# Kernel tuning notes

Measured on AMD Instinct MI355X. Metric: run time of the kernel, lower is better.

## Reference

```python
import jax, jax.numpy as jnp
import numpy as np

B, S, D, H = 512, 200, 512, 8
FF = 1024          # dim_feedforward == hidden_dim
EMB, HID, FIN = 128, 1024, 64
V = 100000
QK_SCALE, ATTN_CLIP, FFN_CLIP, QKV_CLIP = 0.05, 3.0, 2.0, 1.0
PAD = 0


def _ln(x, g, b, eps=1e-6):
    m = jnp.mean(x, -1, keepdims=True)
    v = jnp.mean((x - m) ** 2, -1, keepdims=True)
    return (x - m) / jnp.sqrt(v + eps) * g + b


def setup_inputs() -> dict:
    key = jax.random.key(0)
    ks = jax.random.split(key, 32)
    n = lambda i, shape, s=0.02: (s * jax.random.normal(ks[i], shape)).astype(jnp.float32)
    emb_table = n(0, (V, D)).at[PAD].set(0.0)  # padding row zeroed
    inp = {
        'item_seq': jax.random.randint(ks[20], (B, S), 0, V),
        'user_avg_ctr': jax.random.uniform(ks[21], (B,)),
        'user_total_interactions': jax.random.uniform(ks[22], (B,)),
        'age_price': jax.random.randint(ks[23], (B,), 0, 100),
        'gender_cate': jax.random.randint(ks[24], (B,), 0, 10),
        'cms_group_id': jax.random.randint(ks[25], (B,), 0, 13),
        'emb_table': emb_table,
        'in_proj_w': n(1, (3 * D, D)),
        'out_proj_w': n(2, (D, D)),
        'out_proj_b': jnp.zeros((D,), jnp.float32),
        'ln1_g': jnp.ones((D,), jnp.float32), 'ln1_b': jnp.zeros((D,), jnp.float32),
        'ln2_g': jnp.ones((D,), jnp.float32), 'ln2_b': jnp.zeros((D,), jnp.float32),
        'lin1_w': n(3, (FF, D)), 'lin1_b': jnp.zeros((FF,), jnp.float32),
        'lin2_w': n(4, (D, FF)), 'lin2_b': jnp.zeros((D,), jnp.float32),
        'age_tab': n(5, (100, EMB)), 'gender_tab': n(6, (10, EMB)), 'cms_tab': n(7, (13, EMB)),
        'ctr_w': n(8, (EMB, 1)), 'ctr_b': jnp.zeros((EMB,), jnp.float32),
        'ti_w': n(9, (EMB, 1)), 'ti_b': jnp.zeros((EMB,), jnp.float32),
        'mlp1_w': n(10, (HID, D + 5 * EMB)), 'mlp1_b': jnp.zeros((HID,), jnp.float32),
        'mlp2_w': n(11, (FIN, HID)), 'mlp2_b': jnp.zeros((FIN,), jnp.float32),
    }
    return inp


def reference(item_seq, user_avg_ctr, user_total_interactions, age_price, gender_cate,
              cms_group_id, emb_table, in_proj_w, out_proj_w, out_proj_b,
              ln1_g, ln1_b, ln2_g, ln2_b, lin1_w, lin1_b, lin2_w, lin2_b,
              age_tab, gender_tab, cms_tab, ctr_w, ctr_b, ti_w, ti_b,
              mlp1_w, mlp1_b, mlp2_w, mlp2_b):
    dk = D // H
    pad = item_seq == PAD  # [B,S] key padding mask
    x = jnp.clip(emb_table[item_seq] * 0.5, -1.0, 1.0)  # [B,S,D]

    # ---- custom self-attention block (no in_proj bias, heavy clamping) ----
    qw, kw, vw = in_proj_w[:D], in_proj_w[D:2 * D], in_proj_w[2 * D:]
    q = jnp.clip(x @ qw.T, -QKV_CLIP, QKV_CLIP)
    k = jnp.clip(x @ kw.T, -QKV_CLIP, QKV_CLIP)
    v = jnp.clip(x @ vw.T, -QKV_CLIP, QKV_CLIP)
    q = q.reshape(B, S, H, dk).transpose(0, 2, 1, 3)
    k = k.reshape(B, S, H, dk).transpose(0, 2, 1, 3)
    v = v.reshape(B, S, H, dk).transpose(0, 2, 1, 3)
    scores = jnp.einsum('bhqd,bhkd->bhqk', q, k) / (np.float32(np.sqrt(dk)) * QK_SCALE)
    scores = jnp.clip(scores, -ATTN_CLIP, ATTN_CLIP)
    scores = jnp.where(pad[:, None, None, :], -1e9, scores)
    w = jax.nn.softmax(scores, axis=-1)  # dropout is identity in eval
    x2 = jnp.einsum('bhqk,bhkd->bhqd', w, v).transpose(0, 2, 1, 3).reshape(B, S, D)
    x2 = jnp.clip(x2 @ out_proj_w.T + out_proj_b, -ATTN_CLIP, ATTN_CLIP)
    sa = _ln(x + x2, ln1_g, ln1_b)          # norm1 inside overridden _sa_block
    x = _ln(x + sa, ln1_g, ln1_b)           # base post-norm wraps norm1 again

    # ---- FFN block with clamps ----
    h = jax.nn.relu(jnp.clip(x @ lin1_w.T + lin1_b, -FFN_CLIP, FFN_CLIP))
    f2 = jnp.clip(h @ lin2_w.T + lin2_b, -FFN_CLIP, FFN_CLIP)
    ff = _ln(x + f2, ln2_g, ln2_b)          # norm2 inside overridden _ff_block
    x = _ln(x + ff, ln2_g, ln2_b)           # base wraps norm2 again

    seq_out = jnp.clip(x, -5.0, 5.0)
    m = (~pad).astype(seq_out.dtype)[:, :, None]
    seq_rep = jnp.clip((seq_out * m).sum(1) / (m.sum(1) + 1e-8), -5.0, 5.0)  # [B,D]

    ape = age_tab[age_price]
    ge = gender_tab[gender_cate]
    ce = cms_tab[cms_group_id]
    ctr = user_avg_ctr[:, None] @ ctr_w.T + ctr_b
    ti = user_total_interactions[:, None] @ ti_w.T + ti_b
    u = jnp.concatenate([seq_rep, ctr, ti, ape, ge, ce], axis=-1)  # [B, D+5*EMB]
    return jax.nn.relu(u @ mlp1_w.T + mlp1_b) @ mlp2_w.T + mlp2_b  # [B, FIN]
```

## Files before the change

kernel.cpp:

```cpp
#include <hip/hip_runtime.h>
#include <hip/hip_bf16.h>
#include <stdint.h>

typedef __attribute__((ext_vector_type(8))) short short8;
typedef __attribute__((ext_vector_type(4))) float f32x4;
typedef unsigned short u16;

#define MFMA16(a,b,c) __builtin_amdgcn_mfma_f32_16x16x32_bf16((a),(b),(c),0,0,0)

__device__ __forceinline__ u16 f2bf(float f) {
  unsigned int u = __float_as_uint(f);
  return (u16)((u + 0x7FFFu + ((u >> 16) & 1u)) >> 16);
}
__device__ __forceinline__ float bf2f(u16 h) {
  return __uint_as_float(((unsigned int)h) << 16);
}
__device__ __forceinline__ float clampf(float v, float lo, float hi) {
  return fminf(fmaxf(v, lo), hi);
}
__device__ __forceinline__ void gl2lds16(const u16* g, u16* l) {
  __builtin_amdgcn_global_load_lds(
      (const __attribute__((address_space(1))) unsigned int*)g,
      (__attribute__((address_space(3))) unsigned int*)(uintptr_t)l,
      16, 0, 0);
}

__global__ __launch_bounds__(256) void cvt_bf16_kernel(
    const float* __restrict__ src, u16* __restrict__ dst, int n) {
  for (int i = blockIdx.x*256 + threadIdx.x; i < n; i += gridDim.x*256)
    dst[i] = f2bf(src[i]);
}

__global__ __launch_bounds__(256) void embed_kernel(
    const int* __restrict__ iseq, const float* __restrict__ emb,
    u16* __restrict__ xb) {
  int gid = blockIdx.x*256 + threadIdx.x;
  int m = gid >> 7;
  int c = (gid & 127) * 4;
  int item = iseq[m];
  float4 e = *(const float4*)&emb[(size_t)item*512 + c];
  ushort4 hb;
  hb.x = f2bf(clampf(e.x*0.5f, -1.f, 1.f));
  hb.y = f2bf(clampf(e.y*0.5f, -1.f, 1.f));
  hb.z = f2bf(clampf(e.z*0.5f, -1.f, 1.f));
  hb.w = f2bf(clampf(e.w*0.5f, -1.f, 1.f));
  *(ushort4*)&xb[(size_t)m*512 + c] = hb;
}

__global__ __launch_bounds__(256) void cnt_kernel(
    const int* __restrict__ item_seq, float* __restrict__ cnt) {
  __shared__ int sred[4];
  int b = blockIdx.x, tid = threadIdx.x;
  int lane = tid & 63, wv = tid >> 6;
  int c = 0;
  if (tid < 200) c = (item_seq[b*200 + tid] != 0) ? 1 : 0;
  #pragma unroll
  for (int m = 1; m <= 32; m <<= 1) c += __shfl_xor(c, m);
  if (lane == 0) sred[wv] = c;
  __syncthreads();
  if (tid == 0) cnt[b] = (float)(sred[0]+sred[1]+sred[2]+sred[3]);
}

#define BAR() asm volatile("s_barrier" ::: "memory")

__device__ __forceinline__ void stage_half(const char* gsrc0, size_t rstride,
                                           u16* lhalf, int wv, int lane) {
  #pragma unroll
  for (int j = 0; j < 2; ++j) {
    const int o   = j*8192 + wv*1024 + lane*16;
    const int row = o >> 7;
    const int cb  = (o & 127) ^ ((row & 7) << 4);
    gl2lds16((const u16*)(gsrc0 + (size_t)row*rstride + cb),
             (u16*)((char*)lhalf + j*8192 + wv*1024));
  }
}

__device__ __forceinline__ short8 ldsfrag(const u16* slot, int row, int kb) {
  return *(const short8*)((const char*)slot + row*128 + (kb ^ ((row & 7) << 4)));
}

#define QUAD(AH, NB)                                                          \
  _Pragma("unroll")                                                           \
  for (int i = 0; i < 4; ++i)                                                 \
    _Pragma("unroll")                                                         \
    for (int nf = 0; nf < 2; ++nf)                                            \
      _Pragma("unroll")                                                       \
      for (int ks = 0; ks < 2; ++ks)                                          \
        acc[(AH)*4 + i][(NB)*2 + nf] =                                        \
            MFMA16(af[AH][i][ks], bf[nf][ks], acc[(AH)*4 + i][(NB)*2 + nf]);

template <int MODE>
__global__ __launch_bounds__(512)
void gemm_bt(const u16* __restrict__ A, const u16* __restrict__ Bw,
             const float* __restrict__ bias, int K, int Nt, int swz,
             u16* __restrict__ outB, u16* __restrict__ QKV, long long projStride) {
  __shared__ __align__(16) u16 As[2][256*64];
  __shared__ __align__(16) u16 Bs[2][256*64];
  const int tid  = threadIdx.x;
  const int lane = tid & 63;
  const int wv   = tid >> 6;
  const int wm   = wv >> 2;
  const int wn   = wv & 3;
  const int id   = blockIdx.x;
  int mt, nt2;
  if (swz) { mt = (id / (8*Nt))*8 + (id & 7); nt2 = (id >> 3) % Nt; }
  else     { mt = id / Nt;                    nt2 = id % Nt; }
  const int m0 = mt * 256;
  const int n0 = nt2 * 256;
  const int KT = K >> 6;

  const char* Abase = (const char*)(A  + (size_t)m0*K);
  const char* Bbase = (const char*)(Bw + (size_t)n0*K);
  const size_t rs = (size_t)K * 2;

  const int r16 = lane & 15;
  const int q4  = lane >> 4;

  const f32x4 fz = {0.f, 0.f, 0.f, 0.f};
  f32x4 acc[8][4];
  #pragma unroll
  for (int i = 0; i < 8; ++i)
    #pragma unroll
    for (int j = 0; j < 4; ++j) acc[i][j] = fz;

  stage_half(Abase,            rs, &As[0][0],      wv, lane);
  stage_half(Abase + 128*rs,   rs, &As[0][128*64], wv, lane);
  stage_half(Bbase,            rs, &Bs[0][0],      wv, lane);
  stage_half(Bbase + 128*rs,   rs, &Bs[0][128*64], wv, lane);
  if (KT > 1) {
    stage_half(Abase + 128,          rs, &As[1][0],      wv, lane);
    stage_half(Abase + 128*rs + 128, rs, &As[1][128*64], wv, lane);
    asm volatile("s_waitcnt vmcnt(4)" ::: "memory");
  } else {
    asm volatile("s_waitcnt vmcnt(0)" ::: "memory");
  }
  BAR();

  short8 af[2][4][2];
  short8 bf[2][2];

  for (int t = 0; t < KT; ++t) {
    const int cur = t & 1;
    const u16* Asl = As[cur];
    const u16* Bsl = Bs[cur];
    u16* Bnx = Bs[cur ^ 1];
    u16* Anx = As[cur];
    const char* Bg1 = Bbase + (size_t)(t+1)*128;
    const char* Ag2 = Abase + (size_t)(t+2)*128;
    const bool s1 = (t+1 < KT);
    const bool s2 = (t+2 < KT);

    #pragma unroll
    for (int i = 0; i < 4; ++i)
      #pragma unroll
      for (int ks = 0; ks < 2; ++ks)
        af[0][i][ks] = ldsfrag(Asl, wm*128 + i*16 + r16, ks*64 + q4*16);
    #pragma unroll
    for (int nf = 0; nf < 2; ++nf)
      #pragma unroll
      for (int ks = 0; ks < 2; ++ks)
        bf[nf][ks] = ldsfrag(Bsl, wn*64 + nf*16 + r16, ks*64 + q4*16);
    if (s1) stage_half(Bg1, rs, Bnx, wv, lane);
    BAR();
    __builtin_amdgcn_s_setprio(1);
    QUAD(0, 0);
    __builtin_amdgcn_s_setprio(0);
    BAR();

    #pragma unroll
    for (int i = 0; i < 4; ++i)
      #pragma unroll
      for (int ks = 0; ks < 2; ++ks)
        af[1][i][ks] = ldsfrag(Asl, wm*128 + 64 + i*16 + r16, ks*64 + q4*16);
    if (s1) stage_half(Bg1 + 128*rs, rs, Bnx + 128*64, wv, lane);
    BAR();
    __builtin_amdgcn_s_setprio(1);
    QUAD(1, 0);
    __builtin_amdgcn_s_setprio(0);
    BAR();

    #pragma unroll
    for (int nf = 0; nf < 2; ++nf)
      #pragma unroll
      for (int ks = 0; ks < 2; ++ks)
        bf[nf][ks] = ldsfrag(Bsl, wn*64 + 32 + nf*16 + r16, ks*64 + q4*16);
    if (s2) stage_half(Ag2, rs, Anx, wv, lane);
    BAR();
    __builtin_amdgcn_s_setprio(1);
    QUAD(1, 1);
    __builtin_amdgcn_s_setprio(0);
    BAR();

    if (s2) stage_half(Ag2 + 128*rs, rs, Anx + 128*64, wv, lane);
    if (t < KT-2)       asm volatile("s_waitcnt vmcnt(4)" ::: "memory");
    else if (t == KT-2) asm volatile("s_waitcnt vmcnt(0)" ::: "memory");
    BAR();
    __builtin_amdgcn_s_setprio(1);
    QUAD(0, 1);
    __builtin_amdgcn_s_setprio(0);
    BAR();
  }

  if (MODE == 0) {
    #pragma unroll
    for (int nf = 0; nf < 4; ++nf) {
      const int col = n0 + wn*64 + nf*16 + r16;
      const unsigned proj = (unsigned)col >> 9;
      const unsigned hh   = ((unsigned)col >> 6) & 7u;
      const unsigned dk   = (unsigned)col & 63u;
      u16* base = QKV + (size_t)proj*projStride + (size_t)hh*12800 + dk;
      #pragma unroll
      for (int mi = 0; mi < 8; ++mi) {
        const int rowb = m0 + wm*128 + mi*16 + q4*4;
        int b = rowb / 200;
        int s = rowb - b*200;
        size_t addr = (size_t)b*102400 + (size_t)s*64;
        #pragma unroll
        for (int r = 0; r < 4; ++r) {
          base[addr] = f2bf(clampf(acc[mi][nf][r], -1.f, 1.f));
          ++s; addr += 64;
          if (s == 200) { s = 0; addr += 102400 - 12800; }
        }
      }
    }
  } else {
    const int N = (MODE == 2) ? 1024 : 512;
    #pragma unroll
    for (int nf = 0; nf < 4; ++nf) {
      const int col = n0 + wn*64 + nf*16 + r16;
      const float bvs = bias[col];
      #pragma unroll
      for (int mi = 0; mi < 8; ++mi) {
        const int rowb = m0 + wm*128 + mi*16 + q4*4;
        #pragma unroll
        for (int r = 0; r < 4; ++r) {
          const int row = rowb + r;
          float v = acc[mi][nf][r] + bvs;
          if (MODE == 1)      v = clampf(v, -3.f, 3.f);
          else if (MODE == 2) v = fmaxf(clampf(v, -2.f, 2.f), 0.f);
          else                v = clampf(v, -2.f, 2.f);
          outB[(size_t)row*N + col] = f2bf(v);
        }
      }
    }
  }
}

__global__ __launch_bounds__(512)
void attn_kernel(const u16* __restrict__ Q, const u16* __restrict__ K,
                 const u16* __restrict__ V, const int* __restrict__ iseq,
                 u16* __restrict__ x2b) {
  __shared__ __align__(16) u16 Ks[208*72];
  __shared__ __align__(16) u16 Vs[64*232];
  __shared__ __align__(16) u16 Ps[8][16*40];
  __shared__ float msk[208];

  const int tid = threadIdx.x, lane = tid & 63, wv = tid >> 6;
  const unsigned bid = blockIdx.x;
  const int h = bid & 7;
  const int b = bid >> 3;
  const size_t bh = (size_t)b*8 + h;
  const u16* Kg = K + bh*12800;
  const u16* Vg = V + bh*12800;
  const u16* Qg = Q + bh*12800;

  for (int c = tid; c < 3200; c += 512) {
    int row = c >> 4, q = c & 15;
    *(ushort4*)&Ks[row*72 + q*4] = *(const ushort4*)&Kg[row*64 + q*4];
  }
  {
    const int quad = wv*2 + (lane >> 5);
    const int sl   = lane & 31;
    #pragma unroll
    for (int it = 0; it < 7; ++it) {
      const int s = sl + it*32;
      if (s < 200) {
        ushort4 v4 = *(const ushort4*)&Vg[s*64 + quad*4];
        Vs[(quad*4+0)*232 + s] = v4.x;
        Vs[(quad*4+1)*232 + s] = v4.y;
        Vs[(quad*4+2)*232 + s] = v4.z;
        Vs[(quad*4+3)*232 + s] = v4.w;
      }
    }
  }
  for (int c = tid; c < 2048; c += 512) {
    int dk = c >> 5, s2 = 200 + (c & 31);
    Vs[dk*232 + s2] = 0;
  }
  for (int t = tid; t < 208; t += 512)
    msk[t] = (t < 200 && iseq[b*200 + t] != 0) ? 1.f : 0.f;
  __syncthreads();

  const int colk = lane & 15;
  const int fk8 = (lane >> 4) * 8;
  const int prow = (lane >> 4) * 4;
  const f32x4 fz = {0.f,0.f,0.f,0.f};

  for (int qb = 0; qb < 2; ++qb) {
    const int qrow = qb*128 + wv*16 + (lane & 15);
    const int qsrc = qrow < 200 ? qrow : 199;
    short8 qa0 = *(const short8*)&Qg[(size_t)qsrc*64 + fk8];
    short8 qa1 = *(const short8*)&Qg[(size_t)qsrc*64 + 32 + fk8];
    f32x4 oacc[4];
    #pragma unroll
    for (int nt = 0; nt < 4; ++nt) oacc[nt] = fz;
    float rs[4] = {0.f,0.f,0.f,0.f};

    for (int kt2 = 0; kt2 < 7; ++kt2) {
      #pragma unroll
      for (int half = 0; half < 2; ++half) {
        const int stile = kt2*2 + half;
        if (stile < 13) {
          const int key = stile*16 + colk;
          short8 kb0 = *(const short8*)&Ks[key*72 + fk8];
          short8 kb1 = *(const short8*)&Ks[key*72 + 32 + fk8];
          f32x4 sc = fz;
          __builtin_amdgcn_s_setprio(1);
          sc = MFMA16(qa0, kb0, sc);
          sc = MFMA16(qa1, kb1, sc);
          __builtin_amdgcn_s_setprio(0);
          const float mk = msk[key];
          #pragma unroll
          for (int r = 0; r < 4; ++r) {
            float p = __expf(clampf(sc[r]*2.5f, -3.f, 3.f)) * mk;
            rs[r] += p;
            Ps[wv][(prow + r)*40 + half*16 + colk] = f2bf(p);
          }
        } else {
          #pragma unroll
          for (int r = 0; r < 4; ++r)
            Ps[wv][(prow + r)*40 + half*16 + colk] = 0;
        }
      }
      asm volatile("s_waitcnt lgkmcnt(0)" ::: "memory");
      short8 pa = *(const short8*)&Ps[wv][(lane & 15)*40 + fk8];
      const int kb32 = kt2*32;
      __builtin_amdgcn_s_setprio(1);
      #pragma unroll
      for (int nt = 0; nt < 4; ++nt) {
        short8 vb = *(const short8*)&Vs[(nt*16 + colk)*232 + kb32 + fk8];
        oacc[nt] = MFMA16(pa, vb, oacc[nt]);
      }
      __builtin_amdgcn_s_setprio(0);
      asm volatile("s_waitcnt lgkmcnt(0)" ::: "memory");
    }

    #pragma unroll
    for (int m = 1; m <= 8; m <<= 1)
      #pragma unroll
      for (int r = 0; r < 4; ++r) rs[r] += __shfl_xor(rs[r], m);

    const int srow = qb*128 + wv*16 + prow;
    #pragma unroll
    for (int r = 0; r < 4; ++r) {
      const int s = srow + r;
      if (s < 200) {
        const float inv = rs[r] > 0.f ? 1.f/rs[r] : 0.f;
        const size_t base = ((size_t)b*200 + s)*512 + h*64;
        #pragma unroll
        for (int nt = 0; nt < 4; ++nt)
          x2b[base + nt*16 + colk] = f2bf(oacc[nt][r] * inv);
      }
    }
  }
}

__global__ __launch_bounds__(256)
void ln1_kernel(const u16* __restrict__ xb, const u16* __restrict__ x2b,
                const float* __restrict__ g, const float* __restrict__ bb,
                u16* __restrict__ xnb) {
  const int lane = threadIdx.x & 63, wv = threadIdx.x >> 6;
  const size_t t = (size_t)blockIdx.x*4 + wv;
  const int c0 = lane*4, c1 = 256 + lane*4;
  ushort4 xa = *(const ushort4*)&xb[t*512 + c0];
  ushort4 xc = *(const ushort4*)&xb[t*512 + c1];
  ushort4 ha = *(const ushort4*)&x2b[t*512 + c0];
  ushort4 hc = *(const ushort4*)&x2b[t*512 + c1];
  float xv[8] = {bf2f(xa.x),bf2f(xa.y),bf2f(xa.z),bf2f(xa.w),
                 bf2f(xc.x),bf2f(xc.y),bf2f(xc.z),bf2f(xc.w)};
  float tv[8] = {xv[0]+bf2f(ha.x), xv[1]+bf2f(ha.y), xv[2]+bf2f(ha.z), xv[3]+bf2f(ha.w),
                 xv[4]+bf2f(hc.x), xv[5]+bf2f(hc.y), xv[6]+bf2f(hc.z), xv[7]+bf2f(hc.w)};
  float s1 = 0.f, s2 = 0.f;
  #pragma unroll
  for (int i = 0; i < 8; ++i) { s1 += tv[i]; s2 += tv[i]*tv[i]; }
  #pragma unroll
  for (int m = 1; m <= 32; m <<= 1) { s1 += __shfl_xor(s1, m); s2 += __shfl_xor(s2, m); }
  float mean = s1*(1.f/512.f);
  float inv = 1.f/sqrtf(s2*(1.f/512.f) - mean*mean + 1e-6f);
  float4 ga = *(const float4*)(g + c0), gc = *(const float4*)(g + c1);
  float4 ba = *(const float4*)(bb + c0), bc = *(const float4*)(bb + c1);
  float gv[8] = {ga.x,ga.y,ga.z,ga.w, gc.x,gc.y,gc.z,gc.w};
  float bv[8] = {ba.x,ba.y,ba.z,ba.w, bc.x,bc.y,bc.z,bc.w};
  float uv[8]; float s3 = 0.f, s4 = 0.f;
  #pragma unroll
  for (int i = 0; i < 8; ++i) {
    float sa = (tv[i]-mean)*inv*gv[i] + bv[i];
    uv[i] = xv[i] + sa;
    s3 += uv[i]; s4 += uv[i]*uv[i];
  }
  #pragma unroll
  for (int m = 1; m <= 32; m <<= 1) { s3 += __shfl_xor(s3, m); s4 += __shfl_xor(s4, m); }
  float mean2 = s3*(1.f/512.f);
  float inv2 = 1.f/sqrtf(s4*(1.f/512.f) - mean2*mean2 + 1e-6f);
  ushort4 o0, o1;
  o0.x = f2bf((uv[0]-mean2)*inv2*gv[0] + bv[0]);
  o0.y = f2bf((uv[1]-mean2)*inv2*gv[1] + bv[1]);
  o0.z = f2bf((uv[2]-mean2)*inv2*gv[2] + bv[2]);
  o0.w = f2bf((uv[3]-mean2)*inv2*gv[3] + bv[3]);
  o1.x = f2bf((uv[4]-mean2)*inv2*gv[4] + bv[4]);
  o1.y = f2bf((uv[5]-mean2)*inv2*gv[5] + bv[5]);
  o1.z = f2bf((uv[6]-mean2)*inv2*gv[6] + bv[6]);
  o1.w = f2bf((uv[7]-mean2)*inv2*gv[7] + bv[7]);
  *(ushort4*)&xnb[t*512 + c0] = o0;
  *(ushort4*)&xnb[t*512 + c1] = o1;
}

__global__ __launch_bounds__(256)
void ln2_kernel(const u16* __restrict__ xnb, const u16* __restrict__ f2b,
                const float* __restrict__ g, const float* __restrict__ bb,
                const int* __restrict__ iseq, float* __restrict__ seq_acc) {
  const int tid = threadIdx.x, lane = tid & 63, wv = tid >> 6;
  const int q = blockIdx.x, bl = blockIdx.y;
  const int c8 = lane*8;
  float gv[8], bv[8];
  *(float4*)&gv[0] = *(const float4*)(g + c8);
  *(float4*)&gv[4] = *(const float4*)(g + c8 + 4);
  *(float4*)&bv[0] = *(const float4*)(bb + c8);
  *(float4*)&bv[4] = *(const float4*)(bb + c8 + 4);
  float acc[8] = {};
  for (int i = wv; i < 50; i += 4) {
    const int s = q*50 + i;
    const size_t row = (size_t)bl*200 + s;
    short8 xh = *(const short8*)&xnb[row*512 + c8];
    short8 yh = *(const short8*)&f2b[row*512 + c8];
    float xv[8], tv[8];
    #pragma unroll
    for (int j = 0; j < 8; ++j) {
      xv[j] = bf2f((u16)xh[j]);
      tv[j] = xv[j] + bf2f((u16)yh[j]);
    }
    float s1 = 0.f, s2 = 0.f;
    #pragma unroll
    for (int j = 0; j < 8; ++j) { s1 += tv[j]; s2 += tv[j]*tv[j]; }
    #pragma unroll
    for (int m = 1; m <= 32; m <<= 1) { s1 += __shfl_xor(s1,m); s2 += __shfl_xor(s2,m); }
    float mean = s1*(1.f/512.f);
    float inv = 1.f/sqrtf(s2*(1.f/512.f) - mean*mean + 1e-6f);
    float uv[8]; float s3 = 0.f, s4 = 0.f;
    #pragma unroll
    for (int j = 0; j < 8; ++j) {
      uv[j] = xv[j] + (tv[j]-mean)*inv*gv[j] + bv[j];
      s3 += uv[j]; s4 += uv[j]*uv[j];
    }
    #pragma unroll
    for (int m = 1; m <= 32; m <<= 1) { s3 += __shfl_xor(s3,m); s4 += __shfl_xor(s4,m); }
    float mean2 = s3*(1.f/512.f);
    float inv2 = 1.f/sqrtf(s4*(1.f/512.f) - mean2*mean2 + 1e-6f);
    if (iseq[row] != 0) {
      #pragma unroll
      for (int j = 0; j < 8; ++j)
        acc[j] += clampf((uv[j]-mean2)*inv2*gv[j] + bv[j], -5.f, 5.f);
    }
  }
  float* dst = &seq_acc[(((size_t)bl*4 + q)*4 + wv)*512 + c8];
  *(float4*)&dst[0] = *(float4*)&acc[0];
  *(float4*)&dst[4] = *(float4*)&acc[4];
}

__global__ __launch_bounds__(256)
void build_u_kernel(const float* __restrict__ seq_acc, const float* __restrict__ cnt,
                    const float* __restrict__ uac, const float* __restrict__ uti,
                    const int* __restrict__ age, const int* __restrict__ gen,
                    const int* __restrict__ cms,
                    const float* __restrict__ age_tab, const float* __restrict__ gen_tab,
                    const float* __restrict__ cms_tab,
                    const float* __restrict__ ctr_w, const float* __restrict__ ctr_b,
                    const float* __restrict__ ti_w, const float* __restrict__ ti_b,
                    float* __restrict__ u) {
  const int b = blockIdx.x;
  for (int j = threadIdx.x; j < 1152; j += 256) {
    float v;
    if (j < 512) {
      float ssum = 0.f;
      #pragma unroll
      for (int p = 0; p < 16; ++p) ssum += seq_acc[((size_t)b*16 + p)*512 + j];
      v = clampf(ssum / (cnt[b] + 1e-8f), -5.f, 5.f);
    }
    else if (j < 640)  { int e = j-512;  v = uac[b]*ctr_w[e] + ctr_b[e]; }
    else if (j < 768)  { int e = j-640;  v = uti[b]*ti_w[e] + ti_b[e]; }
    else if (j < 896)  { int e = j-768;  v = age_tab[age[b]*128 + e]; }
    else if (j < 1024) { int e = j-896;  v = gen_tab[gen[b]*128 + e]; }
    else               { int e = j-1024; v = cms_tab[cms[b]*128 + e]; }
    u[(size_t)b*1152 + j] = v;
  }
}

__global__ __launch_bounds__(256)
void mlp1_kernel(const float* __restrict__ u, const float* __restrict__ w,
                 const float* __restrict__ bias, float* __restrict__ h1) {
  __shared__ __align__(16) float As[64][36];
  __shared__ __align__(16) float Wt[32][68];
  const int tid = threadIdx.x;
  const int m0 = blockIdx.x*64, n0 = blockIdx.y*64;
  const int tm = tid >> 4, tn = tid & 15;
  float acc[4][4] = {};
  for (int k0 = 0; k0 < 1152; k0 += 32) {
    for (int c = tid; c < 512; c += 256) {
      int row = c >> 3, q = c & 7;
      *(float4*)&As[row][q*4] = *(const float4*)&u[(size_t)(m0+row)*1152 + k0 + q*4];
      float4 wv4 = *(const float4*)&w[(size_t)(n0+row)*1152 + k0 + q*4];
      Wt[q*4+0][row] = wv4.x; Wt[q*4+1][row] = wv4.y;
      Wt[q*4+2][row] = wv4.z; Wt[q*4+3][row] = wv4.w;
    }
    __syncthreads();
    #pragma unroll
    for (int kk = 0; kk < 32; ++kk) {
      float av[4], bw[4];
      #pragma unroll
      for (int i = 0; i < 4; ++i) av[i] = As[tm*4+i][kk];
      #pragma unroll
      for (int j = 0; j < 4; ++j) bw[j] = Wt[kk][tn*4+j];
      #pragma unroll
      for (int i = 0; i < 4; ++i)
        #pragma unroll
        for (int j = 0; j < 4; ++j) acc[i][j] += av[i]*bw[j];
    }
    __syncthreads();
  }
  #pragma unroll
  for (int i = 0; i < 4; ++i)
    #pragma unroll
    for (int j = 0; j < 4; ++j) {
      int n = n0 + tn*4 + j;
      h1[(size_t)(m0 + tm*4 + i)*1024 + n] = fmaxf(acc[i][j] + bias[n], 0.f);
    }
}

__global__ __launch_bounds__(256)
void mlp2_kernel(const float* __restrict__ h1, const float* __restrict__ w,
                 const float* __restrict__ bias, float* __restrict__ out) {
  const int tid = threadIdx.x;
  const int m = blockIdx.x*4 + (tid >> 6);
  const int n = tid & 63;
  const float4* hr = (const float4*)(h1 + (size_t)m*1024);
  const float4* wr = (const float4*)(w + (size_t)n*1024);
  float acc = 0.f;
  for (int k4 = 0; k4 < 256; ++k4) {
    float4 a = hr[k4], bw = wr[k4];
    acc += a.x*bw.x + a.y*bw.y + a.z*bw.z + a.w*bw.w;
  }
  out[(size_t)m*64 + n] = acc + bias[n];
}

extern "C" void kernel_launch(void* const* d_in, const int* in_sizes, int n_in,
                              void* d_out, int out_size, void* d_ws, size_t ws_size,
                              hipStream_t stream) {
  (void)in_sizes; (void)n_in; (void)out_size;
  const int*   item_seq   = (const int*)d_in[0];
  const float* uac        = (const float*)d_in[1];
  const float* uti        = (const float*)d_in[2];
  const int*   age        = (const int*)d_in[3];
  const int*   gen        = (const int*)d_in[4];
  const int*   cms        = (const int*)d_in[5];
  const float* emb        = (const float*)d_in[6];
  const float* in_proj_w  = (const float*)d_in[7];
  const float* out_proj_w = (const float*)d_in[8];
  const float* out_proj_b = (const float*)d_in[9];
  const float* ln1_g = (const float*)d_in[10];
  const float* ln1_b = (const float*)d_in[11];
  const float* ln2_g = (const float*)d_in[12];
  const float* ln2_b = (const float*)d_in[13];
  const float* lin1_w = (const float*)d_in[14];
  const float* lin1_b = (const float*)d_in[15];
  const float* lin2_w = (const float*)d_in[16];
  const float* lin2_b = (const float*)d_in[17];
  const float* age_tab = (const float*)d_in[18];
  const float* gen_tab = (const float*)d_in[19];
  const float* cms_tab = (const float*)d_in[20];
  const float* ctr_w = (const float*)d_in[21];
  const float* ctr_b = (const float*)d_in[22];
  const float* ti_w  = (const float*)d_in[23];
  const float* ti_b  = (const float*)d_in[24];
  const float* mlp1_w = (const float*)d_in[25];
  const float* mlp1_b = (const float*)d_in[26];
  const float* mlp2_w = (const float*)d_in[27];
  const float* mlp2_b = (const float*)d_in[28];

  const long long TAILB = 25430016LL;
  int CB = 32;
  if      ((long long)ws_size >= 512LL*1024000 + TAILB) CB = 512;
  else if ((long long)ws_size >= 128LL*1024000 + TAILB) CB = 128;
  else if ((long long)ws_size >=  64LL*1024000 + TAILB) CB = 64;
  const long long R = (long long)CB * 204800;

  char* ws = (char*)d_ws;
  u16* xb   = (u16*)(ws);
  u16* x2b  = (u16*)(ws + R);
  u16* Qb   = (u16*)(ws + 2*R);
  u16* Kb   = (u16*)(ws + 3*R);
  u16* Vrb  = (u16*)(ws + 4*R);
  u16* x2o  = Qb;
  u16* xnb  = Kb;
  u16* f2b  = Vrb;
  u16* hbuf = (u16*)(ws);
  char* tail = ws + 5*R;
  float* seq_acc = (float*)(tail);
  float* cnt     = (float*)(tail + 16777216);
  float* u       = (float*)(tail + 16779264);
  float* h1      = (float*)(tail + 19138560);
  u16*   wqkv    = (u16*)(tail + 21235712);
  u16*   wout    = (u16*)(tail + 22808576);
  u16*   wl1     = (u16*)(tail + 23332864);
  u16*   wl2     = (u16*)(tail + 24381440);

  cvt_bf16_kernel<<<768, 256, 0, stream>>>(in_proj_w, wqkv, 1536*512);
  cvt_bf16_kernel<<<256, 256, 0, stream>>>(out_proj_w, wout, 512*512);
  cvt_bf16_kernel<<<512, 256, 0, stream>>>(lin1_w, wl1, 1024*512);
  cvt_bf16_kernel<<<512, 256, 0, stream>>>(lin2_w, wl2, 512*1024);
  cnt_kernel<<<512, 256, 0, stream>>>(item_seq, cnt);

  const int nch = 512 / CB;
  const int Mc  = CB * 200;
  const int Mt  = Mc / 256;
  const int swz = (Mt % 8 == 0) ? 1 : 0;
  const long long projStride = (long long)CB * 102400;
  for (int ch = 0; ch < nch; ++ch) {
    const int* iseq = item_seq + (size_t)ch*CB*200;
    embed_kernel<<<Mc/2, 256, 0, stream>>>(iseq, emb, xb);
    gemm_bt<0><<<Mt*6, 512, 0, stream>>>(xb, wqkv, nullptr, 512, 6, swz,
                                         nullptr, Qb, projStride);
    attn_kernel<<<CB*8, 512, 0, stream>>>(Qb, Kb, Vrb, iseq, x2b);
    gemm_bt<1><<<Mt*2, 512, 0, stream>>>(x2b, wout, out_proj_b, 512, 2, swz,
                                         x2o, nullptr, 0);
    ln1_kernel<<<Mc/4, 256, 0, stream>>>(xb, x2o, ln1_g, ln1_b, xnb);
    gemm_bt<2><<<Mt*4, 512, 0, stream>>>(xnb, wl1, lin1_b, 512, 4, swz,
                                         hbuf, nullptr, 0);
    gemm_bt<3><<<Mt*2, 512, 0, stream>>>(hbuf, wl2, lin2_b, 1024, 2, swz,
                                         f2b, nullptr, 0);
    ln2_kernel<<<dim3(4, CB), 256, 0, stream>>>(xnb, f2b, ln2_g, ln2_b, iseq,
                                                seq_acc + (size_t)ch*CB*8192);
  }

  build_u_kernel<<<512, 256, 0, stream>>>(seq_acc, cnt, uac, uti, age, gen, cms,
                                          age_tab, gen_tab, cms_tab,
                                          ctr_w, ctr_b, ti_w, ti_b, u);
  mlp1_kernel<<<dim3(8, 16), 256, 0, stream>>>(u, mlp1_w, mlp1_b, h1);
  mlp2_kernel<<<128, 256, 0, stream>>>(h1, mlp2_w, mlp2_b, (float*)d_out);
}
```

Before: 1.432 ms.

## Software-pipeline A fragment loads across iterations and halve GEMM barriers

Restructures the bf16 MFMA GEMM main loop. The first A fragments for the next k-tile are now loaded from the other LDS buffer at the end of each iteration, global-to-LDS staging is issued earlier, and the number of s_barriers per k-step drops from eight to four, with sched_barrier fences in between. It also adds a min-blocks hint of 2 to launch_bounds, which tightens the register budget and may cause spills. The next-tile A fragments are read after only a per-wave vmcnt wait and before a barrier, so the code risks reading LDS that other waves have not finished staging.

After: 1.437 ms. No clear change (+0.3%).

```diff
diff --git a/kernel.cpp b/kernel.cpp
--- a/kernel.cpp
+++ b/kernel.cpp
@@ -62,6 +62,7 @@
 }
 
 #define BAR() asm volatile("s_barrier" ::: "memory")
+#define SCHEDB() __builtin_amdgcn_sched_barrier(0)
 
 __device__ __forceinline__ void stage_half(const char* gsrc0, size_t rstride,
                                            u16* lhalf, int wv, int lane) {
@@ -79,18 +80,8 @@
   return *(const short8*)((const char*)slot + row*128 + (kb ^ ((row & 7) << 4)));
 }
 
-#define QUAD(AH, NB)                                                          \
-  _Pragma("unroll")                                                           \
-  for (int i = 0; i < 4; ++i)                                                 \
-    _Pragma("unroll")                                                         \
-    for (int nf = 0; nf < 2; ++nf)                                            \
-      _Pragma("unroll")                                                       \
-      for (int ks = 0; ks < 2; ++ks)                                          \
-        acc[(AH)*4 + i][(NB)*2 + nf] =                                        \
-            MFMA16(af[AH][i][ks], bf[nf][ks], acc[(AH)*4 + i][(NB)*2 + nf]);
-
 template <int MODE>
-__global__ __launch_bounds__(512)
+__global__ __launch_bounds__(512, 2)
 void gemm_bt(const u16* __restrict__ A, const u16* __restrict__ Bw,
              const float* __restrict__ bias, int K, int Nt, int swz,
              u16* __restrict__ outB, u16* __restrict__ QKV, long long projStride) {
@@ -123,6 +114,8 @@
     #pragma unroll
     for (int j = 0; j < 4; ++j) acc[i][j] = fz;
 
+  short8 af0[4][2], af1[4][2], bflo[2][2], bfhi[2][2];
+
   stage_half(Abase,            rs, &As[0][0],      wv, lane);
   stage_half(Abase + 128*rs,   rs, &As[0][128*64], wv, lane);
   stage_half(Bbase,            rs, &Bs[0][0],      wv, lane);
@@ -135,69 +128,108 @@
     asm volatile("s_waitcnt vmcnt(0)" ::: "memory");
   }
   BAR();
-
-  short8 af[2][4][2];
-  short8 bf[2][2];
+  #pragma unroll
+  for (int i = 0; i < 4; ++i)
+    #pragma unroll
+    for (int ks = 0; ks < 2; ++ks)
+      af0[i][ks] = ldsfrag(&As[0][0], wm*128 + i*16 + r16, ks*64 + q4*16);
 
   for (int t = 0; t < KT; ++t) {
     const int cur = t & 1;
     const u16* Asl = As[cur];
     const u16* Bsl = Bs[cur];
-    u16* Bnx = Bs[cur ^ 1];
-    u16* Anx = As[cur];
+    const u16* Asn = As[cur ^ 1];
+    u16* Bnx = (u16*)As[0];
+    Bnx = (u16*)Bs[cur ^ 1];
+    u16* Anx = (u16*)As[cur];
     const char* Bg1 = Bbase + (size_t)(t+1)*128;
     const char* Ag2 = Abase + (size_t)(t+2)*128;
     const bool s1 = (t+1 < KT);
     const bool s2 = (t+2 < KT);
 
+    if (s1) stage_half(Bg1, rs, Bnx, wv, lane);
+    if (t == KT-1) {
+      #pragma unroll
+      for (int i = 0; i < 4; ++i)
+        #pragma unroll
+        for (int ks = 0; ks < 2; ++ks)
+          af0[i][ks] = ldsfrag(Asl, wm*128 + i*16 + r16, ks*64 + q4*16);
+    }
+    #pragma unroll
+    for (int nf = 0; nf < 2; ++nf)
+      #pragma unroll
+      for (int ks = 0; ks < 2; ++ks)
+        bflo[nf][ks] = ldsfrag(Bsl, wn*64 + nf*16 + r16, ks*64 + q4*16);
     #pragma unroll
     for (int i = 0; i < 4; ++i)
       #pragma unroll
       for (int ks = 0; ks < 2; ++ks)
-        af[0][i][ks] = ldsfrag(Asl, wm*128 + i*16 + r16, ks*64 + q4*16);
+        af1[i][ks] = ldsfrag(Asl, wm*128 + 64 + i*16 + r16, ks*64 + q4*16);
+    __builtin_amdgcn_s_setprio(1);
+    #pragma unroll
+    for (int i = 0; i < 4; ++i)
+      #pragma unroll
+      for (int nf = 0; nf < 2; ++nf)
+        #pragma unroll
+        for (int ks = 0; ks < 2; ++ks)
+          acc[i][nf] = MFMA16(af0[i][ks], bflo[nf][ks], acc[i][nf]);
+    __builtin_amdgcn_s_setprio(0);
+    SCHEDB();
+    BAR();
+
+    if (s1) stage_half(Bg1 + 128*rs, rs, Bnx + 128*64, wv, lane);
     #pragma unroll
     for (int nf = 0; nf < 2; ++nf)
       #pragma unroll
       for (int ks = 0; ks < 2; ++ks)
-        bf[nf][ks] = ldsfrag(Bsl, wn*64 + nf*16 + r16, ks*64 + q4*16);
-    if (s1) stage_half(Bg1, rs, Bnx, wv, lane);
+        bfhi[nf][ks] = ldsfrag(Bsl, wn*64 + 32 + nf*16 + r16, ks*64 + q4*16);
+    __builtin_amdgcn_s_setprio(1);
+    #pragma unroll
+    for (int i = 0; i < 4; ++i)
+      #pragma unroll
+      for (int nf = 0; nf < 2; ++nf)
+        #pragma unroll
+        for (int ks = 0; ks < 2; ++ks)
+          acc[4+i][nf] = MFMA16(af1[i][ks], bflo[nf][ks], acc[4+i][nf]);
+    __builtin_amdgcn_s_setprio(0);
+    SCHEDB();
     BAR();
+
+    if (s2) stage_half(Ag2, rs, Anx, wv, lane);
+    if (t < KT-2) asm volatile("s_waitcnt vmcnt(6)" ::: "memory");
     __builtin_amdgcn_s_setprio(1);
-    QUAD(0, 0);
+    #pragma unroll
+    for (int i = 0; i < 4; ++i)
+      #pragma unroll
+      for (int nf = 0; nf < 2; ++nf)
+        #pragma unroll
+        for (int ks = 0; ks < 2; ++ks)
+          acc[4+i][2+nf] = MFMA16(af1[i][ks], bfhi[nf][ks], acc[4+i][2+nf]);
     __builtin_amdgcn_s_setprio(0);
+    SCHEDB();
     BAR();
 
+    if (s2) stage_half(Ag2 + 128*rs, rs, Anx + 128*64, wv, lane);
+    __builtin_amdgcn_s_setprio(1);
     #pragma unroll
     for (int i = 0; i < 4; ++i)
       #pragma unroll
-      for (int ks = 0; ks < 2; ++ks)
-        af[1][i][ks] = ldsfrag(Asl, wm*128 + 64 + i*16 + r16, ks*64 + q4*16);
-    if (s1) stage_half(Bg1 + 128*rs, rs, Bnx + 128*64, wv, lane);
-    BAR();
-    __builtin_amdgcn_s_setprio(1);
-    QUAD(1, 0);
+      for (int nf = 0; nf < 2; ++nf)
+        #pragma unroll
+        for (int ks = 0; ks < 2; ++ks)
+          acc[i][2+nf] = MFMA16(af0[i][ks], bfhi[nf][ks], acc[i][2+nf]);
     __builtin_amdgcn_s_setprio(0);
-    BAR();
-
-    #pragma unroll
-    for (int nf = 0; nf < 2; ++nf)
-      #pragma unroll
-      for (int ks = 0; ks < 2; ++ks)
-        bf[nf][ks] = ldsfrag(Bsl, wn*64 + 32 + nf*16 + r16, ks*64 + q4*16);
-    if (s2) stage_half(Ag2, rs, Anx, wv, lane);
-    BAR();
-    __builtin_amdgcn_s_setprio(1);
-    QUAD(1, 1);
-    __builtin_amdgcn_s_setprio(0);
-    BAR();
-
-    if (s2) stage_half(Ag2 + 128*rs, rs, Anx + 128*64, wv, lane);
-    if (t < KT-2)       asm volatile("s_waitcnt vmcnt(4)" ::: "memory");
-    else if (t == KT-2) asm volatile("s_waitcnt vmcnt(0)" ::: "memory");
-    BAR();
-    __builtin_amdgcn_s_setprio(1);
-    QUAD(0, 1);
-    __builtin_amdgcn_s_setprio(0);
+    if (t < KT-2) {
+      asm volatile("s_waitcnt vmcnt(4)" ::: "memory");
+      #pragma unroll
+      for (int i = 0; i < 4; ++i)
+        #pragma unroll
+        for (int ks = 0; ks < 2; ++ks)
+          af0[i][ks] = ldsfrag(Asn, wm*128 + i*16 + r16, ks*64 + q4*16);
+    } else if (t == KT-2) {
+      asm volatile("s_waitcnt vmcnt(0)" ::: "memory");
+    }
+    SCHEDB();
     BAR();
   }
 
```

## Unroll GEMM K-loop by two with explicit waitcnt scheduling and static buffers

Applied to the files above, without the earlier changes.

Restructures the 8-wave 256x256 GEMM main loop to process two K-tiles per iteration so LDS buffer indices are compile-time constants. It inserts explicit lgkmcnt/vmcnt waits and sched barriers around each MFMA quadrant to interleave LDS reads, global-to-LDS staging and MFMA issue more tightly. It also adds a min-blocks hint to launch_bounds. The unrolled loop assumes KT is even, and the rewritten wait placement risks stalls or races if the vmcnt accounting is off.

After: 1.422 ms. About the same (-0.7%).

```diff
diff --git a/kernel.cpp b/kernel.cpp
--- a/kernel.cpp
+++ b/kernel.cpp
@@ -62,6 +62,10 @@
 }
 
 #define BAR() asm volatile("s_barrier" ::: "memory")
+#define LGKM0() do { asm volatile("s_waitcnt lgkmcnt(0)" ::: "memory"); \
+                     __builtin_amdgcn_sched_barrier(0); } while (0)
+#define VM4() asm volatile("s_waitcnt vmcnt(4)" ::: "memory")
+#define VM0() asm volatile("s_waitcnt vmcnt(0)" ::: "memory")
 
 __device__ __forceinline__ void stage_half(const char* gsrc0, size_t rstride,
                                            u16* lhalf, int wv, int lane) {
@@ -89,8 +93,22 @@
         acc[(AH)*4 + i][(NB)*2 + nf] =                                        \
             MFMA16(af[AH][i][ks], bf[nf][ks], acc[(AH)*4 + i][(NB)*2 + nf]);
 
+#define RD_AF(H, SLOT)                                                        \
+  _Pragma("unroll")                                                           \
+  for (int i = 0; i < 4; ++i)                                                 \
+    _Pragma("unroll")                                                         \
+    for (int ks = 0; ks < 2; ++ks)                                            \
+      af[H][i][ks] = ldsfrag((SLOT), wm*128 + (H)*64 + i*16 + r16, ks*64 + q4*16);
+
+#define RD_BF(SLOT, OFF)                                                      \
+  _Pragma("unroll")                                                           \
+  for (int nf = 0; nf < 2; ++nf)                                              \
+    _Pragma("unroll")                                                         \
+    for (int ks = 0; ks < 2; ++ks)                                            \
+      bf[nf][ks] = ldsfrag((SLOT), wn*64 + (OFF) + nf*16 + r16, ks*64 + q4*16);
+
 template <int MODE>
-__global__ __launch_bounds__(512)
+__global__ __launch_bounds__(512, 2)
 void gemm_bt(const u16* __restrict__ A, const u16* __restrict__ Bw,
              const float* __restrict__ bias, int K, int Nt, int swz,
              u16* __restrict__ outB, u16* __restrict__ QKV, long long projStride) {
@@ -108,6 +126,7 @@
   const int m0 = mt * 256;
   const int n0 = nt2 * 256;
   const int KT = K >> 6;
+  const int NI = KT >> 1;
 
   const char* Abase = (const char*)(A  + (size_t)m0*K);
   const char* Bbase = (const char*)(Bw + (size_t)n0*K);
@@ -123,82 +142,74 @@
     #pragma unroll
     for (int j = 0; j < 4; ++j) acc[i][j] = fz;
 
-  stage_half(Abase,            rs, &As[0][0],      wv, lane);
-  stage_half(Abase + 128*rs,   rs, &As[0][128*64], wv, lane);
-  stage_half(Bbase,            rs, &Bs[0][0],      wv, lane);
-  stage_half(Bbase + 128*rs,   rs, &Bs[0][128*64], wv, lane);
-  if (KT > 1) {
-    stage_half(Abase + 128,          rs, &As[1][0],      wv, lane);
-    stage_half(Abase + 128*rs + 128, rs, &As[1][128*64], wv, lane);
-    asm volatile("s_waitcnt vmcnt(4)" ::: "memory");
-  } else {
-    asm volatile("s_waitcnt vmcnt(0)" ::: "memory");
-  }
-  BAR();
-
   short8 af[2][4][2];
   short8 bf[2][2];
 
-  for (int t = 0; t < KT; ++t) {
-    const int cur = t & 1;
-    const u16* Asl = As[cur];
-    const u16* Bsl = Bs[cur];
-    u16* Bnx = Bs[cur ^ 1];
-    u16* Anx = As[cur];
-    const char* Bg1 = Bbase + (size_t)(t+1)*128;
-    const char* Ag2 = Abase + (size_t)(t+2)*128;
-    const bool s1 = (t+1 < KT);
-    const bool s2 = (t+2 < KT);
-
-    #pragma unroll
-    for (int i = 0; i < 4; ++i)
-      #pragma unroll
-      for (int ks = 0; ks < 2; ++ks)
-        af[0][i][ks] = ldsfrag(Asl, wm*128 + i*16 + r16, ks*64 + q4*16);
-    #pragma unroll
-    for (int nf = 0; nf < 2; ++nf)
-      #pragma unroll
-      for (int ks = 0; ks < 2; ++ks)
-        bf[nf][ks] = ldsfrag(Bsl, wn*64 + nf*16 + r16, ks*64 + q4*16);
-    if (s1) stage_half(Bg1, rs, Bnx, wv, lane);
+  stage_half(Abase,              rs, &As[0][0],      wv, lane);
+  stage_half(Abase + 128*rs,     rs, &As[0][128*64], wv, lane);
+  stage_half(Bbase,              rs, &Bs[0][0],      wv, lane);
+  stage_half(Bbase + 128*rs,     rs, &Bs[0][128*64], wv, lane);
+  stage_half(Abase + 128,        rs, &As[1][0],      wv, lane);
+  stage_half(Abase + 128*rs + 128, rs, &As[1][128*64], wv, lane);
+  VM4();
+  BAR();
+
+  for (int it = 0; it < NI; ++it) {
+    const int ta = it*2;
+    const bool m2 = (ta + 2 < KT);
+    const char* gBb  = Bbase + (size_t)(ta+1)*128;
+    const char* gAa2 = Abase + (size_t)(ta+2)*128;
+    const char* gBa2 = Bbase + (size_t)(ta+2)*128;
+    const char* gAb1 = Abase + (size_t)(ta+3)*128;
+
+    RD_AF(0, As[0]); RD_BF(Bs[0], 0);
+    asm volatile("s_waitcnt lgkmcnt(8)" ::: "memory");
+    stage_half(gBb, rs, &Bs[1][0], wv, lane);
+    BAR(); LGKM0();
+    __builtin_amdgcn_s_setprio(1); QUAD(0, 0); __builtin_amdgcn_s_setprio(0);
+    VM4(); BAR();
+
+    RD_AF(1, As[0]);
+    stage_half(gBb + 128*rs, rs, &Bs[1][128*64], wv, lane);
+    BAR(); LGKM0();
+    __builtin_amdgcn_s_setprio(1); QUAD(1, 0); __builtin_amdgcn_s_setprio(0);
+    VM4(); BAR();
+
+    RD_BF(Bs[0], 32);
+    if (m2) stage_half(gAa2, rs, &As[0][0], wv, lane);
+    BAR(); LGKM0();
+    __builtin_amdgcn_s_setprio(1); QUAD(1, 1); __builtin_amdgcn_s_setprio(0);
+    VM4(); BAR();
+
+    if (m2) stage_half(gAa2 + 128*rs, rs, &As[0][128*64], wv, lane);
     BAR();
-    __builtin_amdgcn_s_setprio(1);
-    QUAD(0, 0);
-    __builtin_amdgcn_s_setprio(0);
+    __builtin_amdgcn_s_setprio(1); QUAD(0, 1); __builtin_amdgcn_s_setprio(0);
+    if (m2) { VM4(); } else { VM0(); }
     BAR();
 
-    #pragma unroll
-    for (int i = 0; i < 4; ++i)
-      #pragma unroll
-      for (int ks = 0; ks < 2; ++ks)
-        af[1][i][ks] = ldsfrag(Asl, wm*128 + 64 + i*16 + r16, ks*64 + q4*16);
-    if (s1) stage_half(Bg1 + 128*rs, rs, Bnx + 128*64, wv, lane);
+    RD_AF(0, As[1]); RD_BF(Bs[1], 0);
+    asm volatile("s_waitcnt lgkmcnt(8)" ::: "memory");
+    if (m2) stage_half(gBa2, rs, &Bs[0][0], wv, lane);
+    BAR(); LGKM0();
+    __builtin_amdgcn_s_setprio(1); QUAD(0, 0); __builtin_amdgcn_s_setprio(0);
+    VM4(); BAR();
+
+    RD_AF(1, As[1]);
+    if (m2) stage_half(gBa2 + 128*rs, rs, &Bs[0][128*64], wv, lane);
+    BAR(); LGKM0();
+    __builtin_amdgcn_s_setprio(1); QUAD(1, 0); __builtin_amdgcn_s_setprio(0);
+    VM4(); BAR();
+
+    RD_BF(Bs[1], 32);
+    if (m2) stage_half(gAb1, rs, &As[1][0], wv, lane);
+    BAR(); LGKM0();
+    __builtin_amdgcn_s_setprio(1); QUAD(1, 1); __builtin_amdgcn_s_setprio(0);
+    VM4(); BAR();
+
+    if (m2) stage_half(gAb1 + 128*rs, rs, &As[1][128*64], wv, lane);
     BAR();
-    __builtin_amdgcn_s_setprio(1);
-    QUAD(1, 0);
-    __builtin_amdgcn_s_setprio(0);
-    BAR();
-
-    #pragma unroll
-    for (int nf = 0; nf < 2; ++nf)
-      #pragma unroll
-      for (int ks = 0; ks < 2; ++ks)
-        bf[nf][ks] = ldsfrag(Bsl, wn*64 + 32 + nf*16 + r16, ks*64 + q4*16);
-    if (s2) stage_half(Ag2, rs, Anx, wv, lane);
-    BAR();
-    __builtin_amdgcn_s_setprio(1);
-    QUAD(1, 1);
-    __builtin_amdgcn_s_setprio(0);
-    BAR();
-
-    if (s2) stage_half(Ag2 + 128*rs, rs, Anx + 128*64, wv, lane);
-    if (t < KT-2)       asm volatile("s_waitcnt vmcnt(4)" ::: "memory");
-    else if (t == KT-2) asm volatile("s_waitcnt vmcnt(0)" ::: "memory");
-    BAR();
-    __builtin_amdgcn_s_setprio(1);
-    QUAD(0, 1);
-    __builtin_amdgcn_s_setprio(0);
-    BAR();
+    __builtin_amdgcn_s_setprio(1); QUAD(0, 1); __builtin_amdgcn_s_setprio(0);
+    VM4(); BAR();
   }
 
   if (MODE == 0) {
```
